# Performance work log

Hardware: AMD Instinct MI355X
Metric: run time of the kernel (lower is better)

The kernel has to match this reference:

```python
import jax, jax.numpy as jnp
import numpy as np

D_MODEL = 1024
NUM_HEADS = 16
HEAD_WIDTH = 64
SEQ_LEN = 2048
BATCH = 2
NEG_INF = -1e9


def alibi_slopes(num_heads):
    # 2**(-i * 8/num_heads) for i = 1..num_heads, shape [H, 1, 1]
    step = 8.0 / num_heads
    i = jnp.arange(1, num_heads + 1, dtype=jnp.float32)
    return (2.0 ** (-i * step))[:, None, None]


def relative_positions(t_q, t_v):
    # matrix[i, j] = j - i, shape [t_q, t_v]
    return (jnp.arange(t_v)[None, :] - jnp.arange(t_q)[:, None]).astype(jnp.float32)


def setup_inputs() -> dict:
    key = jax.random.key(0)
    ks = jax.random.split(key, 6)
    queries = jax.random.normal(ks[0], (BATCH, SEQ_LEN, D_MODEL), dtype=jnp.float32)
    keys = jax.random.normal(ks[1], (BATCH, SEQ_LEN, D_MODEL), dtype=jnp.float32)
    values = jax.random.normal(ks[2], (BATCH, SEQ_LEN, D_MODEL), dtype=jnp.float32)
    # causal additive mask, broadcastable [1, 1, S, S]
    causal = jnp.where(
        jnp.arange(SEQ_LEN)[None, :] > jnp.arange(SEQ_LEN)[:, None], NEG_INF, 0.0
    ).astype(jnp.float32)[None, None]
    scale = 1.0 / np.sqrt(D_MODEL)
    Wq = jax.random.normal(ks[3], (D_MODEL, D_MODEL), dtype=jnp.float32) * scale
    Wk = jax.random.normal(ks[4], (D_MODEL, D_MODEL), dtype=jnp.float32) * scale
    Wv = jax.random.normal(ks[5], (D_MODEL, D_MODEL), dtype=jnp.float32) * scale
    return {"queries": queries, "keys": keys, "values": values, "mask": causal,
            "Wq": Wq, "Wk": Wk, "Wv": Wv}


def reference(queries, keys, values, mask, Wq, Wk, Wv):
    N, t_q, d = queries.shape
    _, t_v, _ = keys.shape
    H, hw = NUM_HEADS, HEAD_WIDTH

    def split_heads(x, t):
        # [N, t, d] -> [N, H, t, hw]  (nn.Linear: x @ W.T)
        return x.reshape(N, t, H, hw).transpose(0, 2, 1, 3)

    q = split_heads(queries @ Wq.T, t_q)
    k = split_heads(keys @ Wk.T, t_v)
    v = split_heads(values @ Wv.T, t_v)

    att = jnp.einsum("bhqd,bhkd->bhqk", q, k) / np.sqrt(hw)
    # ALiBi bias: slope_h * (j - i), broadcast over batch
    att = att + (alibi_slopes(H) * relative_positions(t_q, t_v))[None]
    att = att + mask[:, :, :t_q, :t_v]
    att = jax.nn.softmax(att, axis=-1)
    res = jnp.einsum("bhqk,bhkd->bhqd", att, v)  # [N, H, t_q, hw]
    return res.transpose(0, 2, 1, 3).reshape(N, t_v, d)
```

## Files before the change

### kernel.cpp

```cpp
#include <hip/hip_runtime.h>
#include <hip/hip_bf16.h>

#define BATCH 2
#define HEADS 16
#define SEQ 2048
#define HW 64
#define DMODEL 1024

typedef unsigned short u16;
typedef __attribute__((ext_vector_type(8))) short short8;
typedef __attribute__((ext_vector_type(4))) float floatx4;

typedef __attribute__((address_space(3))) void* lds_t;
typedef const __attribute__((address_space(1))) void* gbl_t;

__device__ __forceinline__ u16 f2bf(float f) {
    union { float f; unsigned int u; } v; v.f = f;
    unsigned int r = v.u + 0x7fffu + ((v.u >> 16) & 1u);
    return (u16)(r >> 16);
}

__device__ __forceinline__ unsigned int pk2bf(float a, float b) {
    union { __hip_bfloat162 h; unsigned int u; } c;
    c.h = __float22bfloat162_rn(make_float2(a, b));
    return c.u;
}

__global__ __launch_bounds__(256) void convw_kernel(
    const float* __restrict__ wk, const float* __restrict__ wv, const float* __restrict__ wq,
    u16* __restrict__ ok, u16* __restrict__ ov, u16* __restrict__ oq)
{
    const int z = blockIdx.y;
    const float* src; u16* dst; float mul = 1.0f;
    if (z == 0)      { src = wk; dst = ok; }
    else if (z == 1) { src = wv; dst = ov; }
    else             { src = wq; dst = oq; mul = 0.125f; }

    const int i = (blockIdx.x * 256 + threadIdx.x) * 8;
    float4 a = *reinterpret_cast<const float4*>(src + i);
    float4 b = *reinterpret_cast<const float4*>(src + i + 4);
    uint4 o;
    o.x = pk2bf(a.x * mul, a.y * mul);
    o.y = pk2bf(a.z * mul, a.w * mul);
    o.z = pk2bf(b.x * mul, b.y * mul);
    o.w = pk2bf(b.z * mul, b.w * mul);
    *reinterpret_cast<uint4*>(dst + i) = o;
}

__global__ __launch_bounds__(256) void proj_kernel(
    const float* __restrict__ Xk, const float* __restrict__ Xv, const float* __restrict__ Xq,
    const u16* __restrict__ Wb,
    u16* __restrict__ Ok, u16* __restrict__ Ov, u16* __restrict__ Oq)
{
    const int bid = blockIdx.x;
    const int xcd = bid & 7, idx = bid >> 3;
    const int z = idx >> 5;
    const int r = idx & 31;
    const int tm = (xcd << 2) | (r >> 3);
    const int tn = r & 7;

    const float* X = (z == 0) ? Xk : (z == 1) ? Xv : Xq;
    const u16* W = Wb + (size_t)z * DMODEL * DMODEL;

    __shared__ u16 As[128][72];
    __shared__ u16 Bs[128][64];

    const int tid = threadIdx.x;
    const int lane = tid & 63, wave = tid >> 6;
    const int quad = lane >> 4, l15 = lane & 15;
    const int swz = l15 & 7;
    const int wm = (wave >> 1) << 6, wn = (wave & 1) << 6;

    const int sr = tid >> 4;
    const int sc = (tid & 15) << 2;
    const float* Xp = X + (size_t)(tm * 128 + sr) * DMODEL + sc;

    const int srowB = (wave << 5) + (lane >> 3);
    const int scolB = (((lane & 7) ^ (lane >> 3)) << 3);
    const u16* gB = W + (size_t)(tn * 128 + srowB) * DMODEL + scolB;

    float4 ra[8];
#define PLOAD(K0) \
    for (int i = 0; i < 8; i++) \
        ra[i] = *reinterpret_cast<const float4*>(Xp + (size_t)16 * i * DMODEL + (K0));

    floatx4 acc[4][4];
    for (int i = 0; i < 4; i++) for (int j = 0; j < 4; j++) acc[i][j] = (floatx4)0.0f;

    PLOAD(0);
    for (int k0 = 0; k0 < DMODEL; k0 += 64) {
        for (int j = 0; j < 4; j++)
            __builtin_amdgcn_global_load_lds((gbl_t)(gB + (size_t)j * 8 * DMODEL + k0),
                (lds_t)(&Bs[(wave << 5) + (j << 3)][0]), 16, 0, 0);
        for (int i = 0; i < 8; i++) {
            uint2 pa; pa.x = pk2bf(ra[i].x, ra[i].y); pa.y = pk2bf(ra[i].z, ra[i].w);
            *reinterpret_cast<uint2*>(&As[sr + 16 * i][sc]) = pa;
        }
        __syncthreads();
        if (k0 + 64 < DMODEL) { PLOAD(k0 + 64); }
        for (int kc = 0; kc < 2; kc++) {
            short8 af[4], bf[4];
            for (int i = 0; i < 4; i++)
                af[i] = *reinterpret_cast<const short8*>(&As[wm + i * 16 + l15][kc * 32 + quad * 8]);
            for (int j = 0; j < 4; j++)
                bf[j] = *reinterpret_cast<const short8*>(&Bs[wn + j * 16 + l15][((kc * 4 + quad) ^ swz) << 3]);
            for (int i = 0; i < 4; i++)
                for (int j = 0; j < 4; j++)
                    acc[i][j] = __builtin_amdgcn_mfma_f32_16x16x32_bf16(af[i], bf[j], acc[i][j], 0, 0, 0);
        }
        __syncthreads();
    }
#undef PLOAD

    if (z != 1) {
        u16* O = (z == 0) ? Ok : Oq;
        for (int i = 0; i < 4; i++) for (int j = 0; j < 4; j++) {
            int n = (tn << 7) + wn + (j << 4) + l15;
            int h = n >> 6, d = n & 63;
            for (int rr = 0; rr < 4; rr++) {
                int m = (tm << 7) + wm + (i << 4) + (quad << 2) + rr;
                int b = m >> 11, s = m & 2047;
                int pc = (((d >> 3) ^ (s & 7)) << 3) | (d & 7);
                O[(size_t)((((b << 4) + h) << 11) + s) * 64 + pc] = f2bf(acc[i][j][rr]);
            }
        }
    } else {
        for (int i = 0; i < 4; i++) for (int j = 0; j < 4; j++) {
            int n = (tn << 7) + wn + (j << 4) + l15;
            int h = n >> 6, d = n & 63;
            int m = (tm << 7) + wm + (i << 4) + (quad << 2);
            int b = m >> 11, s0 = m & 2047;
            int ps = (s0 & ~63) | (((((s0 >> 3) & 7) ^ (d & 7)) << 3)) | (s0 & 7);
            uint2 pk;
            pk.x = pk2bf(acc[i][j][0], acc[i][j][1]);
            pk.y = pk2bf(acc[i][j][2], acc[i][j][3]);
            *reinterpret_cast<uint2*>(Ov + ((size_t)(((b << 4) + h) << 6) + d) * SEQ + ps) = pk;
        }
    }
}

__global__ __launch_bounds__(256) void attn_kernel(
    const u16* __restrict__ Qg, const u16* __restrict__ K,
    const u16* __restrict__ VtG, float* __restrict__ out)
{
    __shared__ u16 smem[16896];
    u16* Pst = smem + 12288;

    const int tid = threadIdx.x;
    const int lane = tid & 63, wave = tid >> 6;
    const int quad = lane >> 4, l15 = lane & 15;

    const int bid = blockIdx.x;
    const int qt = 31 - (bid >> 5);
    const int bh = bid & 31;
    const int b = bh >> 4, h = bh & 15;
    const float slope = exp2f(-0.5f * (float)(h + 1));
    const int q0 = qt << 6;
    const int swz = l15 & 7;

    const u16* Qh  = Qg  + (size_t)bh * SEQ * HW;
    const u16* Kh  = K   + (size_t)bh * SEQ * HW;
    const u16* Vth = VtG + (size_t)bh * HW * SEQ;

#define ISSUE_K(KV, BUF) do { \
    const u16* gk_ = Kh + (size_t)((KV) + wave * 16) * 64 + lane * 8; \
    __builtin_amdgcn_global_load_lds((gbl_t)gk_, (lds_t)(smem + (BUF) * 4096 + wave * 1024), 16, 0, 0); \
    __builtin_amdgcn_global_load_lds((gbl_t)(gk_ + 512), (lds_t)(smem + (BUF) * 4096 + wave * 1024 + 512), 16, 0, 0); \
} while (0)
#define ISSUE_V(KV) do { \
    const u16* gv_ = Vth + (size_t)(wave * 16 + (lane >> 3)) * SEQ + (KV) + (lane & 7) * 8; \
    __builtin_amdgcn_global_load_lds((gbl_t)gv_, (lds_t)(smem + 8192 + wave * 1024), 16, 0, 0); \
    __builtin_amdgcn_global_load_lds((gbl_t)(gv_ + 8 * SEQ), (lds_t)(smem + 8192 + wave * 1024 + 512), 16, 0, 0); \
} while (0)

    {
        const u16* gq = Qh + (size_t)(q0 + wave * 16) * 64 + lane * 8;
        __builtin_amdgcn_global_load_lds((gbl_t)gq, (lds_t)(smem + 8192 + wave * 1024), 16, 0, 0);
        __builtin_amdgcn_global_load_lds((gbl_t)(gq + 512), (lds_t)(smem + 8192 + wave * 1024 + 512), 16, 0, 0);
    }
    asm volatile("s_waitcnt vmcnt(0)" ::: "memory");
    short8 qf[2];
    qf[0] = *reinterpret_cast<const short8*>(smem + 8192 + (wave * 16 + l15) * 64 + ((quad ^ swz) << 3));
    qf[1] = *reinterpret_cast<const short8*>(smem + 8192 + (wave * 16 + l15) * 64 + (((quad + 4) ^ swz) << 3));
    asm volatile("s_waitcnt lgkmcnt(0)" ::: "memory");
    __builtin_amdgcn_sched_barrier(0);

    ISSUE_K(0, 0);

    const float L2E = 1.44269504088896340736f;
    const float MB  = 12.0f * L2E;
    const int qg = q0 + (wave << 4) + l15;
    const float SL = slope * L2E;

    float lpart = 0.0f;
    floatx4 acc_o[4];
    for (int t = 0; t < 4; t++) acc_o[t] = (floatx4)0.0f;

    for (int kt = 0; kt <= qt; kt++) {
        const int kv0 = kt << 6;
        asm volatile("s_waitcnt vmcnt(0)" ::: "memory");
        __builtin_amdgcn_s_barrier();
        __builtin_amdgcn_sched_barrier(0);
        ISSUE_V(kv0);
        if (kt < qt) { ISSUE_K(kv0 + 64, (kt + 1) & 1); }

        const u16* Kbase = smem + (kt & 1) * 4096;
        floatx4 sv[4];
        __builtin_amdgcn_s_setprio(1);
        for (int t = 0; t < 4; t++) {
            short8 kf0 = *reinterpret_cast<const short8*>(Kbase + (t * 16 + l15) * 64 + ((quad ^ swz) << 3));
            short8 kf1 = *reinterpret_cast<const short8*>(Kbase + (t * 16 + l15) * 64 + (((quad + 4) ^ swz) << 3));
            floatx4 s = (floatx4)0.0f;
            s = __builtin_amdgcn_mfma_f32_16x16x32_bf16(kf0, qf[0], s, 0, 0, 0);
            s = __builtin_amdgcn_mfma_f32_16x16x32_bf16(kf1, qf[1], s, 0, 0, 0);
            sv[t] = s;
        }
        __builtin_amdgcn_s_setprio(0);

        u16* Pt = Pst + wave * 1152;
        if (kt < qt) {
            const float b0 = fmaf(SL, (float)(kv0 + (quad << 2) - qg), -MB);
            for (int t = 0; t < 4; t++) {
                float p0 = __builtin_amdgcn_exp2f(fmaf(sv[t][0], L2E, fmaf(SL, (float)(t * 16 + 0), b0)));
                float p1 = __builtin_amdgcn_exp2f(fmaf(sv[t][1], L2E, fmaf(SL, (float)(t * 16 + 1), b0)));
                float p2 = __builtin_amdgcn_exp2f(fmaf(sv[t][2], L2E, fmaf(SL, (float)(t * 16 + 2), b0)));
                float p3 = __builtin_amdgcn_exp2f(fmaf(sv[t][3], L2E, fmaf(SL, (float)(t * 16 + 3), b0)));
                lpart += (p0 + p1) + (p2 + p3);
                uint2 pk; pk.x = pk2bf(p0, p1); pk.y = pk2bf(p2, p3);
                *reinterpret_cast<uint2*>(Pt + l15 * 72 + t * 16 + (quad << 2)) = pk;
            }
        } else {
            const float fb = (float)(kv0 + (quad << 2) - qg);
            for (int t = 0; t < 4; t++) {
                float p[4];
                for (int r = 0; r < 4; r++) {
                    float rel = fb + (float)(t * 16 + r);
                    float bd = fmaf(fminf(slope * rel, -1e9f * rel), L2E, -MB);
                    p[r] = __builtin_amdgcn_exp2f(fmaf(sv[t][r], L2E, bd));
                }
                lpart += (p[0] + p[1]) + (p[2] + p[3]);
                uint2 pk; pk.x = pk2bf(p[0], p[1]); pk.y = pk2bf(p[2], p[3]);
                *reinterpret_cast<uint2*>(Pt + l15 * 72 + t * 16 + (quad << 2)) = pk;
            }
        }

        if (kt < qt) { asm volatile("s_waitcnt vmcnt(2)" ::: "memory"); }
        else         { asm volatile("s_waitcnt vmcnt(0)" ::: "memory"); }
        __builtin_amdgcn_s_barrier();
        __builtin_amdgcn_sched_barrier(0);

        short8 pf0 = *reinterpret_cast<const short8*>(Pt + l15 * 72 + quad * 8);
        short8 pf1 = *reinterpret_cast<const short8*>(Pt + l15 * 72 + 32 + quad * 8);
        __builtin_amdgcn_s_setprio(1);
        for (int t2 = 0; t2 < 4; t2++) {
            short8 vf0 = *reinterpret_cast<const short8*>(smem + 8192 + (t2 * 16 + l15) * 64 + ((quad ^ swz) << 3));
            short8 vf1 = *reinterpret_cast<const short8*>(smem + 8192 + (t2 * 16 + l15) * 64 + (((quad + 4) ^ swz) << 3));
            acc_o[t2] = __builtin_amdgcn_mfma_f32_16x16x32_bf16(vf0, pf0, acc_o[t2], 0, 0, 0);
            acc_o[t2] = __builtin_amdgcn_mfma_f32_16x16x32_bf16(vf1, pf1, acc_o[t2], 0, 0, 0);
        }
        __builtin_amdgcn_s_setprio(0);
    }
#undef ISSUE_K
#undef ISSUE_V

    float l_run = lpart;
    l_run += __shfl_xor(l_run, 16);
    l_run += __shfl_xor(l_run, 32);
    const float inv = 1.0f / l_run;

    float* op = out + (size_t)(b * SEQ + qg) * DMODEL + h * 64;
    for (int t2 = 0; t2 < 4; t2++) {
        float4 o;
        o.x = acc_o[t2][0] * inv; o.y = acc_o[t2][1] * inv;
        o.z = acc_o[t2][2] * inv; o.w = acc_o[t2][3] * inv;
        *reinterpret_cast<float4*>(op + t2 * 16 + (quad << 2)) = o;
    }
}

extern "C" void kernel_launch(void* const* d_in, const int* in_sizes, int n_in,
                              void* d_out, int out_size, void* d_ws, size_t ws_size,
                              hipStream_t stream) {
    const float* q  = (const float*)d_in[0];
    const float* k  = (const float*)d_in[1];
    const float* v  = (const float*)d_in[2];
    const float* wq = (const float*)d_in[4];
    const float* wk = (const float*)d_in[5];
    const float* wv = (const float*)d_in[6];
    float* out = (float*)d_out;

    const size_t he = (size_t)BATCH * HEADS * SEQ * HW;
    const size_t we = (size_t)DMODEL * DMODEL;
    u16* Kb  = (u16*)d_ws;
    u16* VtB = Kb + he;
    u16* Qb  = VtB + he;

    u16* Wb = (u16*)d_out;
    convw_kernel<<<dim3(512, 3), 256, 0, stream>>>(wk, wv, wq, Wb, Wb + we, Wb + 2 * we);
    proj_kernel<<<768, 256, 0, stream>>>(k, v, q, Wb, Kb, VtB, Qb);
    attn_kernel<<<BATCH * HEADS * (SEQ / 64), 256, 0, stream>>>(Qb, Kb, VtB, out);
}
```

Measured before the change: 184.6 us.

## Double-buffer weight tiles in projection GEMM with async LDS prefetch

New measurement: 193.2 us. +4.7%, slower.

```diff
diff --git a/kernel.cpp b/kernel.cpp
--- a/kernel.cpp
+++ b/kernel.cpp
@@ -63,7 +63,7 @@
     const u16* W = Wb + (size_t)z * DMODEL * DMODEL;
 
     __shared__ u16 As[128][72];
-    __shared__ u16 Bs[128][64];
+    __shared__ u16 Bs[2][128][64];
 
     const int tid = threadIdx.x;
     const int lane = tid & 63, wave = tid >> 6;
@@ -83,34 +83,49 @@
 #define PLOAD(K0) \
     for (int i = 0; i < 8; i++) \
         ra[i] = *reinterpret_cast<const float4*>(Xp + (size_t)16 * i * DMODEL + (K0));
+#define ISSUE_B(K0, BUF) \
+    for (int j = 0; j < 4; j++) \
+        __builtin_amdgcn_global_load_lds((gbl_t)(gB + (size_t)j * 8 * DMODEL + (K0)), \
+            (lds_t)(&Bs[BUF][(wave << 5) + (j << 3)][0]), 16, 0, 0);
 
     floatx4 acc[4][4];
     for (int i = 0; i < 4; i++) for (int j = 0; j < 4; j++) acc[i][j] = (floatx4)0.0f;
 
     PLOAD(0);
-    for (int k0 = 0; k0 < DMODEL; k0 += 64) {
-        for (int j = 0; j < 4; j++)
-            __builtin_amdgcn_global_load_lds((gbl_t)(gB + (size_t)j * 8 * DMODEL + k0),
-                (lds_t)(&Bs[(wave << 5) + (j << 3)][0]), 16, 0, 0);
+    ISSUE_B(0, 0);
+
+    for (int kt = 0; kt < 16; kt++) {
+        const int cur = kt & 1;
         for (int i = 0; i < 8; i++) {
             uint2 pa; pa.x = pk2bf(ra[i].x, ra[i].y); pa.y = pk2bf(ra[i].z, ra[i].w);
             *reinterpret_cast<uint2*>(&As[sr + 16 * i][sc]) = pa;
         }
-        __syncthreads();
-        if (k0 + 64 < DMODEL) { PLOAD(k0 + 64); }
+        if (kt < 15) {
+            PLOAD((kt + 1) * 64);
+            ISSUE_B((kt + 1) * 64, cur ^ 1);
+            asm volatile("s_waitcnt vmcnt(12)" ::: "memory");
+        } else {
+            asm volatile("s_waitcnt vmcnt(0)" ::: "memory");
+        }
+        asm volatile("s_waitcnt lgkmcnt(0)" ::: "memory");
+        __builtin_amdgcn_s_barrier();
+        __builtin_amdgcn_sched_barrier(0);
+
         for (int kc = 0; kc < 2; kc++) {
             short8 af[4], bf[4];
             for (int i = 0; i < 4; i++)
                 af[i] = *reinterpret_cast<const short8*>(&As[wm + i * 16 + l15][kc * 32 + quad * 8]);
             for (int j = 0; j < 4; j++)
-                bf[j] = *reinterpret_cast<const short8*>(&Bs[wn + j * 16 + l15][((kc * 4 + quad) ^ swz) << 3]);
+                bf[j] = *reinterpret_cast<const short8*>(&Bs[cur][wn + j * 16 + l15][((kc * 4 + quad) ^ swz) << 3]);
             for (int i = 0; i < 4; i++)
                 for (int j = 0; j < 4; j++)
                     acc[i][j] = __builtin_amdgcn_mfma_f32_16x16x32_bf16(af[i], bf[j], acc[i][j], 0, 0, 0);
         }
-        __syncthreads();
+        __builtin_amdgcn_s_barrier();
+        __builtin_amdgcn_sched_barrier(0);
     }
 #undef PLOAD
+#undef ISSUE_B
 
     if (z != 1) {
         u16* O = (z == 0) ? Ok : Oq;
```
